# Optimization experiments

Measured on AMD Instinct MI355X. Metric: run time of the kernel, lower is better.

Reference implementation:

```python
import jax, jax.numpy as jnp
import numpy as np

V, E, H, A, S, B = 32000, 1024, 1024, 10, 512, 64


def setup_inputs() -> dict:
    key = jax.random.key(0)
    ks = jax.random.split(key, 12)
    s = 0.02
    return {
        "dec_input": jax.random.randint(ks[0], (B, 1), 0, V, dtype=jnp.int32),
        "dec_hidden": jax.random.normal(ks[1], (1, B, H), jnp.float32),
        "enc_outputs": jax.random.normal(ks[2], (S, B, H), jnp.float32),
        "emb": jax.random.normal(ks[3], (V, E), jnp.float32) * s,
        "Wa1": jax.random.normal(ks[4], (A, 2 * H), jnp.float32) * s,  # attention layer 1, no bias
        "Wa2": jax.random.normal(ks[5], (1, A), jnp.float32) * s,      # attention layer 2, no bias
        "W_ih": jax.random.normal(ks[6], (3 * H, E + H), jnp.float32) * s,  # GRU input weights (r,z,n)
        "W_hh": jax.random.normal(ks[7], (3 * H, H), jnp.float32) * s,      # GRU hidden weights (r,z,n)
        "b_ih": jnp.zeros((3 * H,), jnp.float32),
        "b_hh": jnp.zeros((3 * H,), jnp.float32),
        "W_out": jax.random.normal(ks[8], (V, H), jnp.float32) * s,
        "b_out": jnp.zeros((V,), jnp.float32),
    }


def reference(dec_input, dec_hidden, enc_outputs, emb, Wa1, Wa2, W_ih, W_hh, b_ih, b_hh, W_out, b_out):
    h_last = dec_hidden[-1]  # [B, H]
    # Bahdanau additive attention over encoder time steps (axis 0)
    hh = jnp.broadcast_to(h_last[None], enc_outputs.shape)        # [S, B, H]
    feats = jnp.concatenate([hh, enc_outputs], axis=-1)           # [S, B, 2H]
    e = jnp.tanh(feats @ Wa1.T) @ Wa2.T                           # [S, B, 1]
    alpha = jax.nn.softmax(e, axis=0)                             # softmax over seq
    c = jnp.sum(alpha * enc_outputs, axis=0)                      # [B, H]
    # embedding lookup for the single decoder step
    x = emb[dec_input[:, 0]]                                      # [B, E]
    xc = jnp.concatenate([x, c], axis=1)                          # [B, E+H]
    # single-step GRU (PyTorch gate order: r, z, n)
    gi = xc @ W_ih.T + b_ih                                       # [B, 3H]
    gh = h_last @ W_hh.T + b_hh                                   # [B, 3H]
    i_r, i_z, i_n = jnp.split(gi, 3, axis=1)
    h_r, h_z, h_n = jnp.split(gh, 3, axis=1)
    r = jax.nn.sigmoid(i_r + h_r)
    z = jax.nn.sigmoid(i_z + h_z)
    n = jnp.tanh(i_n + r * h_n)
    h_new = (1.0 - z) * n + z * h_last                            # [B, H]
    logits = h_new @ W_out.T + b_out                              # [B, V]
    return logits, h_new[None]                                    # ([B,V], [1,B,H])
```

## Files before the change

kernel.cpp:

```cpp
#include <hip/hip_runtime.h>
#include <math.h>

#define Vv 32000
#define Ee 1024
#define Hh 1024
#define Aa 10
#define Ss 512
#define Bb 64

typedef __attribute__((ext_vector_type(8))) short bf16x8;
typedef __attribute__((ext_vector_type(4))) short s16x4;
typedef __attribute__((ext_vector_type(4))) float f32x4;

__device__ inline short f2bf(float f) {
    union { float f; unsigned int u; } v;
    v.f = f;
    unsigned int r = (v.u + 0x7FFFu + ((v.u >> 16) & 1u)) >> 16;
    return (short)r;
}

__device__ inline bf16x8 cvt8(float4 lo, float4 hi) {
    bf16x8 r;
    r[0] = f2bf(lo.x); r[1] = f2bf(lo.y); r[2] = f2bf(lo.z); r[3] = f2bf(lo.w);
    r[4] = f2bf(hi.x); r[5] = f2bf(hi.y); r[6] = f2bf(hi.z); r[7] = f2bf(hi.w);
    return r;
}

__global__ __launch_bounds__(256) void hpart_kernel(const float* __restrict__ Wa1,
                                                    const float* __restrict__ h,
                                                    float* __restrict__ hpart) {
    __shared__ float red[256];
    const int b = blockIdx.x, t = threadIdx.x;
    float p[Aa];
#pragma unroll
    for (int a = 0; a < Aa; a++) p[a] = 0.f;
    for (int k = t; k < Hh; k += 256) {
        float hv = h[b * Hh + k];
#pragma unroll
        for (int a = 0; a < Aa; a++) p[a] += Wa1[a * (2 * Hh) + k] * hv;
    }
    for (int a = 0; a < Aa; a++) {
        red[t] = p[a];
        __syncthreads();
        for (int o = 128; o > 0; o >>= 1) {
            if (t < o) red[t] += red[t + o];
            __syncthreads();
        }
        if (t == 0) hpart[b * 16 + a] = red[0];
        __syncthreads();
    }
}

__global__ __launch_bounds__(256) void scores_kernel(const float* __restrict__ enc,
                                                     const float* __restrict__ Wa1,
                                                     const float* __restrict__ Wa2,
                                                     const float* __restrict__ hpart,
                                                     float* __restrict__ e_out) {
    __shared__ float es[64][65];
    __shared__ float red[4][64][11];
    const int t = threadIdx.x;
    const int m0 = blockIdx.x * 64;
    const int q = __builtin_amdgcn_readfirstlane((int)(t >> 6));
    const int lane = t & 63;
    const float4* enc4 = (const float4*)enc;

    float acc[Aa];
#pragma unroll
    for (int a = 0; a < Aa; a++) acc[a] = 0.f;

    for (int c = 0; c < 16; c++) {
#pragma unroll
        for (int p = 0; p < 4; p++) {
            int idx = t + p * 256;
            int r = idx >> 4, kq = idx & 15;
            float4 v = enc4[(size_t)(m0 + r) * 256 + c * 16 + kq];
            es[r][kq * 4 + 0] = v.x;
            es[r][kq * 4 + 1] = v.y;
            es[r][kq * 4 + 2] = v.z;
            es[r][kq * 4 + 3] = v.w;
        }
        __syncthreads();
        const int kbase = Hh + c * 64 + q * 16;
#pragma unroll
        for (int j = 0; j < 16; j++) {
            float ev = es[lane][q * 16 + j];
#pragma unroll
            for (int a = 0; a < Aa; a++)
                acc[a] += Wa1[a * (2 * Hh) + kbase + j] * ev;
        }
        __syncthreads();
    }
#pragma unroll
    for (int a = 0; a < Aa; a++) red[q][lane][a] = acc[a];
    __syncthreads();
    if (t < 64) {
        float ev = 0.f;
#pragma unroll
        for (int a = 0; a < Aa; a++) {
            float tot = red[0][t][a] + red[1][t][a] + red[2][t][a] + red[3][t][a]
                        + hpart[t * 16 + a];
            ev += Wa2[a] * tanhf(tot);
        }
        e_out[m0 + t] = ev;
    }
}

__global__ __launch_bounds__(512) void softmax_kernel(const float* __restrict__ e,
                                                      float* __restrict__ alpha) {
    __shared__ float red[512];
    const int b = blockIdx.x, s = threadIdx.x;
    float v = e[s * Bb + b];
    red[s] = v;
    __syncthreads();
    for (int o = 256; o > 0; o >>= 1) {
        if (s < o) red[s] = fmaxf(red[s], red[s + o]);
        __syncthreads();
    }
    float m = red[0];
    __syncthreads();
    float ex = expf(v - m);
    red[s] = ex;
    __syncthreads();
    for (int o = 256; o > 0; o >>= 1) {
        if (s < o) red[s] += red[s + o];
        __syncthreads();
    }
    float inv = 1.f / red[0];
    alpha[s * Bb + b] = ex * inv;
}

__global__ __launch_bounds__(128) void context_kernel(const float* __restrict__ enc,
                                                      const float* __restrict__ alpha,
                                                      float* __restrict__ c) {
    const int b = blockIdx.x, hc = blockIdx.y, sc = blockIdx.z;
    const int h4 = hc * 128 + threadIdx.x;
    const float4* enc4 = (const float4*)enc;
    float4 acc = {0.f, 0.f, 0.f, 0.f};
    const int s0 = sc * 128;
    for (int s = s0; s < s0 + 128; ++s) {
        float a = alpha[s * Bb + b];
        float4 ev = enc4[(size_t)(s * Bb + b) * 256 + h4];
        acc.x += a * ev.x;
        acc.y += a * ev.y;
        acc.z += a * ev.z;
        acc.w += a * ev.w;
    }
    float* cp = c + b * Hh + h4 * 4;
    atomicAdd(cp + 0, acc.x);
    atomicAdd(cp + 1, acc.y);
    atomicAdd(cp + 2, acc.z);
    atomicAdd(cp + 3, acc.w);
}

__global__ __launch_bounds__(256) void xc_kernel(const int* __restrict__ dec_input,
                                                 const float* __restrict__ emb,
                                                 const float* __restrict__ c,
                                                 const float* __restrict__ h,
                                                 short* __restrict__ xcb,
                                                 short* __restrict__ hb) {
    const int b = blockIdx.x, t = threadIdx.x;
    const int tok = dec_input[b];
    float4 ev = ((const float4*)(emb + (size_t)tok * Ee))[t];
    float4 cv = ((const float4*)(c + (size_t)b * Hh))[t];
    float4 hv = ((const float4*)(h + (size_t)b * Hh))[t];
    s16x4 e4 = {f2bf(ev.x), f2bf(ev.y), f2bf(ev.z), f2bf(ev.w)};
    s16x4 c4 = {f2bf(cv.x), f2bf(cv.y), f2bf(cv.z), f2bf(cv.w)};
    s16x4 h4 = {f2bf(hv.x), f2bf(hv.y), f2bf(hv.z), f2bf(hv.w)};
    ((s16x4*)(xcb + (size_t)b * 2048))[t] = e4;
    ((s16x4*)(xcb + (size_t)b * 2048 + 1024))[t] = c4;
    ((s16x4*)(hb + (size_t)b * 1024))[t] = h4;
}

__global__ __launch_bounds__(256) void gemm_mfma_kernel(
    const short* __restrict__ Abf,
    const float* __restrict__ W,
    const float* __restrict__ bias,
    float* __restrict__ C,
    int N, int K, int Klen, int doAtomic) {
    const int t = threadIdx.x;
    const int w = t >> 6, lane = t & 63;
    const int col = lane & 15, quad = lane >> 4;
    const int n0 = blockIdx.x * 64 + w * 16;
    const int kb0 = blockIdx.y * Klen;

    f32x4 acc[4];
#pragma unroll
    for (int mt = 0; mt < 4; mt++) acc[mt] = (f32x4){0.f, 0.f, 0.f, 0.f};

    const float* wrow = W + (size_t)(n0 + col) * K + kb0 + quad * 8;
    const short* arow = Abf + (size_t)col * K + kb0 + quad * 8;

    for (int kb = 0; kb < Klen; kb += 64) {
        float4 w0 = *(const float4*)(wrow + kb);
        float4 w1 = *(const float4*)(wrow + kb + 4);
        float4 w2 = *(const float4*)(wrow + kb + 32);
        float4 w3 = *(const float4*)(wrow + kb + 36);
        bf16x8 bf0 = cvt8(w0, w1);
        bf16x8 bf1 = cvt8(w2, w3);
        bf16x8 a0[4], a1[4];
#pragma unroll
        for (int mt = 0; mt < 4; mt++) {
            a0[mt] = *(const bf16x8*)(arow + (size_t)mt * 16 * K + kb);
            a1[mt] = *(const bf16x8*)(arow + (size_t)mt * 16 * K + kb + 32);
        }
#pragma unroll
        for (int mt = 0; mt < 4; mt++)
            acc[mt] = __builtin_amdgcn_mfma_f32_16x16x32_bf16(a0[mt], bf0, acc[mt], 0, 0, 0);
#pragma unroll
        for (int mt = 0; mt < 4; mt++)
            acc[mt] = __builtin_amdgcn_mfma_f32_16x16x32_bf16(a1[mt], bf1, acc[mt], 0, 0, 0);
    }

    const float bv = (bias != nullptr) ? bias[n0 + col] : 0.f;
#pragma unroll
    for (int mt = 0; mt < 4; mt++) {
#pragma unroll
        for (int r = 0; r < 4; r++) {
            int m = mt * 16 + quad * 4 + r;
            size_t off = (size_t)m * N + n0 + col;
            if (doAtomic) atomicAdd(&C[off], acc[mt][r]);
            else C[off] = acc[mt][r] + bv;
        }
    }
}

__global__ __launch_bounds__(256) void gru_kernel(const float* __restrict__ gi,
                                                  const float* __restrict__ gh,
                                                  const float* __restrict__ b_ih,
                                                  const float* __restrict__ b_hh,
                                                  const float* __restrict__ h,
                                                  float* __restrict__ h_new,
                                                  short* __restrict__ hnb) {
    const int idx = blockIdx.x * 256 + threadIdx.x;
    const int b = idx >> 10, j = idx & 1023;
    const size_t base = (size_t)b * (3 * Hh);
    float ir = gi[base + j] + b_ih[j];
    float iz = gi[base + Hh + j] + b_ih[Hh + j];
    float in_ = gi[base + 2 * Hh + j] + b_ih[2 * Hh + j];
    float hr = gh[base + j] + b_hh[j];
    float hz = gh[base + Hh + j] + b_hh[Hh + j];
    float hn = gh[base + 2 * Hh + j] + b_hh[2 * Hh + j];
    float r = 1.f / (1.f + expf(-(ir + hr)));
    float z = 1.f / (1.f + expf(-(iz + hz)));
    float n = tanhf(in_ + r * hn);
    float val = (1.f - z) * n + z * h[idx];
    h_new[idx] = val;
    hnb[idx] = f2bf(val);
}

extern "C" void kernel_launch(void* const* d_in, const int* in_sizes, int n_in,
                              void* d_out, int out_size, void* d_ws, size_t ws_size,
                              hipStream_t stream) {
    const int* dec_input = (const int*)d_in[0];
    const float* dec_hidden = (const float*)d_in[1];
    const float* enc = (const float*)d_in[2];
    const float* emb = (const float*)d_in[3];
    const float* Wa1 = (const float*)d_in[4];
    const float* Wa2 = (const float*)d_in[5];
    const float* W_ih = (const float*)d_in[6];
    const float* W_hh = (const float*)d_in[7];
    const float* b_ih = (const float*)d_in[8];
    const float* b_hh = (const float*)d_in[9];
    const float* W_out = (const float*)d_in[10];
    const float* b_out = (const float*)d_in[11];

    float* out = (float*)d_out;
    float* logits = out;
    float* h_new = out + (size_t)Bb * Vv;

    float* ws = (float*)d_ws;
    float* e_ptr = ws;
    float* alpha_ptr = ws + 32768;
    float* hpart_ptr = ws + 65536;
    float* c_ptr = ws + 66560;
    float* gi_ptr = ws + 132096;
    float* gh_ptr = ws + 328704;
    short* xcb_ptr = (short*)(ws + 525312);
    short* hb_ptr = (short*)(ws + 590848);
    short* hnb_ptr = (short*)(ws + 623616);

    hipMemsetAsync(c_ptr, 0, (size_t)Bb * Hh * sizeof(float), stream);
    hipMemsetAsync(gi_ptr, 0, (size_t)2 * Bb * 3 * Hh * sizeof(float), stream);

    hpart_kernel<<<Bb, 256, 0, stream>>>(Wa1, dec_hidden, hpart_ptr);
    scores_kernel<<<(Ss * Bb) / 64, 256, 0, stream>>>(enc, Wa1, Wa2, hpart_ptr, e_ptr);
    softmax_kernel<<<Bb, 512, 0, stream>>>(e_ptr, alpha_ptr);
    context_kernel<<<dim3(Bb, 2, 4), 128, 0, stream>>>(enc, alpha_ptr, c_ptr);
    xc_kernel<<<Bb, 256, 0, stream>>>(dec_input, emb, c_ptr, dec_hidden, xcb_ptr, hb_ptr);

    gemm_mfma_kernel<<<dim3(3 * Hh / 64, 8), 256, 0, stream>>>(
        xcb_ptr, W_ih, nullptr, gi_ptr, 3 * Hh, Ee + Hh, 256, 1);
    gemm_mfma_kernel<<<dim3(3 * Hh / 64, 4), 256, 0, stream>>>(
        hb_ptr, W_hh, nullptr, gh_ptr, 3 * Hh, Hh, 256, 1);

    gru_kernel<<<(Bb * Hh) / 256, 256, 0, stream>>>(gi_ptr, gh_ptr, b_ih, b_hh,
                                                    dec_hidden, h_new, hnb_ptr);

    gemm_mfma_kernel<<<dim3(Vv / 64, 1), 256, 0, stream>>>(
        hnb_ptr, W_out, b_out, logits, Vv, Hh, 1024, 0);
}
```

Measured before the change: 481.6 us.

## Use MFMA for attention scores and replace atomics with split-K partial buffers

The attention score projection (enc @ Wa1 encoder half) now runs on bf16 MFMA with two K-splits, and the tanh/Wa2 combine moves into the softmax kernel. Context and GRU GEMMs write split partials to workspace buffers instead of using atomicAdd, so the memsets go away and the reductions happen in xc_kernel and gru_kernel. The aim is to cut the scalar FMA cost of the scores pass and the atomic traffic, at the cost of bf16 rounding in the scores, extra partial-buffer reads, and workspace regions reused across stages.

Result: faster. 448.0 us (-7.0%).

```diff
diff --git a/kernel.cpp b/kernel.cpp
--- a/kernel.cpp
+++ b/kernel.cpp
@@ -7,6 +7,7 @@
 #define Aa 10
 #define Ss 512
 #define Bb 64
+#define Mm (Ss * Bb)
 
 typedef __attribute__((ext_vector_type(8))) short bf16x8;
 typedef __attribute__((ext_vector_type(4))) short s16x4;
@@ -51,74 +52,67 @@
     }
 }
 
-__global__ __launch_bounds__(256) void scores_kernel(const float* __restrict__ enc,
-                                                     const float* __restrict__ Wa1,
-                                                     const float* __restrict__ Wa2,
-                                                     const float* __restrict__ hpart,
-                                                     float* __restrict__ e_out) {
-    __shared__ float es[64][65];
-    __shared__ float red[4][64][11];
+__global__ __launch_bounds__(256) void scores_mfma_kernel(
+    const float* __restrict__ enc,
+    const float* __restrict__ Wa1,
+    float* __restrict__ epre) {
     const int t = threadIdx.x;
-    const int m0 = blockIdx.x * 64;
-    const int q = __builtin_amdgcn_readfirstlane((int)(t >> 6));
-    const int lane = t & 63;
-    const float4* enc4 = (const float4*)enc;
-
-    float acc[Aa];
-#pragma unroll
-    for (int a = 0; a < Aa; a++) acc[a] = 0.f;
-
+    const int w = t >> 6, lane = t & 63;
+    const int col = lane & 15, quad = lane >> 4;
+    const int m0 = (blockIdx.x * 4 + w) * 16;
+    const int p = blockIdx.y;
+    const int kb0 = p * 512;
+
+    f32x4 acc = {0.f, 0.f, 0.f, 0.f};
+    const int wa_row = (col < Aa) ? col : 0;
+    const float* wrow = Wa1 + (size_t)wa_row * (2 * Hh) + Hh + kb0 + quad * 8;
+    const float* arow = enc + (size_t)(m0 + col) * Hh + kb0 + quad * 8;
+    const bool valid = (col < Aa);
+
+#pragma unroll
     for (int c = 0; c < 16; c++) {
-#pragma unroll
-        for (int p = 0; p < 4; p++) {
-            int idx = t + p * 256;
-            int r = idx >> 4, kq = idx & 15;
-            float4 v = enc4[(size_t)(m0 + r) * 256 + c * 16 + kq];
-            es[r][kq * 4 + 0] = v.x;
-            es[r][kq * 4 + 1] = v.y;
-            es[r][kq * 4 + 2] = v.z;
-            es[r][kq * 4 + 3] = v.w;
+        float4 a0 = *(const float4*)(arow + c * 32);
+        float4 a1 = *(const float4*)(arow + c * 32 + 4);
+        bf16x8 af = cvt8(a0, a1);
+        bf16x8 bf;
+        if (valid) {
+            float4 b0 = *(const float4*)(wrow + c * 32);
+            float4 b1 = *(const float4*)(wrow + c * 32 + 4);
+            bf = cvt8(b0, b1);
+        } else {
+            bf = (bf16x8){0, 0, 0, 0, 0, 0, 0, 0};
         }
-        __syncthreads();
-        const int kbase = Hh + c * 64 + q * 16;
-#pragma unroll
-        for (int j = 0; j < 16; j++) {
-            float ev = es[lane][q * 16 + j];
-#pragma unroll
-            for (int a = 0; a < Aa; a++)
-                acc[a] += Wa1[a * (2 * Hh) + kbase + j] * ev;
-        }
-        __syncthreads();
-    }
-#pragma unroll
-    for (int a = 0; a < Aa; a++) red[q][lane][a] = acc[a];
-    __syncthreads();
-    if (t < 64) {
-        float ev = 0.f;
-#pragma unroll
-        for (int a = 0; a < Aa; a++) {
-            float tot = red[0][t][a] + red[1][t][a] + red[2][t][a] + red[3][t][a]
-                        + hpart[t * 16 + a];
-            ev += Wa2[a] * tanhf(tot);
-        }
-        e_out[m0 + t] = ev;
-    }
-}
-
-__global__ __launch_bounds__(512) void softmax_kernel(const float* __restrict__ e,
+        acc = __builtin_amdgcn_mfma_f32_16x16x32_bf16(af, bf, acc, 0, 0, 0);
+    }
+    float* out = epre + ((size_t)p * Mm + m0) * 16;
+#pragma unroll
+    for (int r = 0; r < 4; r++)
+        out[(quad * 4 + r) * 16 + col] = acc[r];
+}
+
+__global__ __launch_bounds__(512) void softmax_kernel(const float* __restrict__ epre,
+                                                      const float* __restrict__ hpart,
+                                                      const float* __restrict__ Wa2,
                                                       float* __restrict__ alpha) {
     __shared__ float red[512];
     const int b = blockIdx.x, s = threadIdx.x;
-    float v = e[s * Bb + b];
+    const int m = s * Bb + b;
+    float v = 0.f;
+#pragma unroll
+    for (int a = 0; a < Aa; a++) {
+        float tot = hpart[b * 16 + a] + epre[(size_t)m * 16 + a]
+                    + epre[((size_t)Mm + m) * 16 + a];
+        v += Wa2[a] * tanhf(tot);
+    }
     red[s] = v;
     __syncthreads();
     for (int o = 256; o > 0; o >>= 1) {
         if (s < o) red[s] = fmaxf(red[s], red[s + o]);
         __syncthreads();
     }
-    float m = red[0];
+    float mx = red[0];
     __syncthreads();
-    float ex = expf(v - m);
+    float ex = expf(v - mx);
     red[s] = ex;
     __syncthreads();
     for (int o = 256; o > 0; o >>= 1) {
@@ -129,15 +123,15 @@
     alpha[s * Bb + b] = ex * inv;
 }
 
-__global__ __launch_bounds__(128) void context_kernel(const float* __restrict__ enc,
+__global__ __launch_bounds__(256) void context_kernel(const float* __restrict__ enc,
                                                       const float* __restrict__ alpha,
-                                                      float* __restrict__ c) {
-    const int b = blockIdx.x, hc = blockIdx.y, sc = blockIdx.z;
-    const int h4 = hc * 128 + threadIdx.x;
+                                                      float* __restrict__ cpart) {
+    const int b = blockIdx.x, sc = blockIdx.y;
+    const int h4 = threadIdx.x;
     const float4* enc4 = (const float4*)enc;
     float4 acc = {0.f, 0.f, 0.f, 0.f};
-    const int s0 = sc * 128;
-    for (int s = s0; s < s0 + 128; ++s) {
+    const int s0 = sc * 32;
+    for (int s = s0; s < s0 + 32; ++s) {
         float a = alpha[s * Bb + b];
         float4 ev = enc4[(size_t)(s * Bb + b) * 256 + h4];
         acc.x += a * ev.x;
@@ -145,30 +139,31 @@
         acc.z += a * ev.z;
         acc.w += a * ev.w;
     }
-    float* cp = c + b * Hh + h4 * 4;
-    atomicAdd(cp + 0, acc.x);
-    atomicAdd(cp + 1, acc.y);
-    atomicAdd(cp + 2, acc.z);
-    atomicAdd(cp + 3, acc.w);
+    ((float4*)cpart)[((size_t)sc * Bb + b) * 256 + h4] = acc;
 }
 
 __global__ __launch_bounds__(256) void xc_kernel(const int* __restrict__ dec_input,
                                                  const float* __restrict__ emb,
-                                                 const float* __restrict__ c,
+                                                 const float* __restrict__ cpart,
                                                  const float* __restrict__ h,
                                                  short* __restrict__ xcb,
                                                  short* __restrict__ hb) {
     const int b = blockIdx.x, t = threadIdx.x;
     const int tok = dec_input[b];
+    float4 cv = {0.f, 0.f, 0.f, 0.f};
+#pragma unroll
+    for (int p = 0; p < 16; p++) {
+        float4 v = ((const float4*)cpart)[((size_t)p * Bb + b) * 256 + t];
+        cv.x += v.x; cv.y += v.y; cv.z += v.z; cv.w += v.w;
+    }
     float4 ev = ((const float4*)(emb + (size_t)tok * Ee))[t];
-    float4 cv = ((const float4*)(c + (size_t)b * Hh))[t];
     float4 hv = ((const float4*)(h + (size_t)b * Hh))[t];
     s16x4 e4 = {f2bf(ev.x), f2bf(ev.y), f2bf(ev.z), f2bf(ev.w)};
     s16x4 c4 = {f2bf(cv.x), f2bf(cv.y), f2bf(cv.z), f2bf(cv.w)};
-    s16x4 h4 = {f2bf(hv.x), f2bf(hv.y), f2bf(hv.z), f2bf(hv.w)};
+    s16x4 h4v = {f2bf(hv.x), f2bf(hv.y), f2bf(hv.z), f2bf(hv.w)};
     ((s16x4*)(xcb + (size_t)b * 2048))[t] = e4;
     ((s16x4*)(xcb + (size_t)b * 2048 + 1024))[t] = c4;
-    ((s16x4*)(hb + (size_t)b * 1024))[t] = h4;
+    ((s16x4*)(hb + (size_t)b * 1024))[t] = h4v;
 }
 
 __global__ __launch_bounds__(256) void gemm_mfma_kernel(
@@ -176,7 +171,7 @@
     const float* __restrict__ W,
     const float* __restrict__ bias,
     float* __restrict__ C,
-    int N, int K, int Klen, int doAtomic) {
+    int N, int K, int Klen) {
     const int t = threadIdx.x;
     const int w = t >> 6, lane = t & 63;
     const int col = lane & 15, quad = lane >> 4;
@@ -212,20 +207,19 @@
     }
 
     const float bv = (bias != nullptr) ? bias[n0 + col] : 0.f;
+    float* Cp = C + (size_t)blockIdx.y * 64 * N;
 #pragma unroll
     for (int mt = 0; mt < 4; mt++) {
 #pragma unroll
         for (int r = 0; r < 4; r++) {
             int m = mt * 16 + quad * 4 + r;
-            size_t off = (size_t)m * N + n0 + col;
-            if (doAtomic) atomicAdd(&C[off], acc[mt][r]);
-            else C[off] = acc[mt][r] + bv;
+            Cp[(size_t)m * N + n0 + col] = acc[mt][r] + bv;
         }
     }
 }
 
-__global__ __launch_bounds__(256) void gru_kernel(const float* __restrict__ gi,
-                                                  const float* __restrict__ gh,
+__global__ __launch_bounds__(256) void gru_kernel(const float* __restrict__ gip,
+                                                  const float* __restrict__ ghp,
                                                   const float* __restrict__ b_ih,
                                                   const float* __restrict__ b_hh,
                                                   const float* __restrict__ h,
@@ -234,12 +228,18 @@
     const int idx = blockIdx.x * 256 + threadIdx.x;
     const int b = idx >> 10, j = idx & 1023;
     const size_t base = (size_t)b * (3 * Hh);
-    float ir = gi[base + j] + b_ih[j];
-    float iz = gi[base + Hh + j] + b_ih[Hh + j];
-    float in_ = gi[base + 2 * Hh + j] + b_ih[2 * Hh + j];
-    float hr = gh[base + j] + b_hh[j];
-    float hz = gh[base + Hh + j] + b_hh[Hh + j];
-    float hn = gh[base + 2 * Hh + j] + b_hh[2 * Hh + j];
+    float ir = b_ih[j], iz = b_ih[Hh + j], in_ = b_ih[2 * Hh + j];
+    float hr = b_hh[j], hz = b_hh[Hh + j], hn = b_hh[2 * Hh + j];
+#pragma unroll
+    for (int p = 0; p < 8; p++) {
+        const float* g = gip + (size_t)p * Bb * 3 * Hh + base;
+        ir += g[j]; iz += g[Hh + j]; in_ += g[2 * Hh + j];
+    }
+#pragma unroll
+    for (int p = 0; p < 8; p++) {
+        const float* g = ghp + (size_t)p * Bb * 3 * Hh + base;
+        hr += g[j]; hz += g[Hh + j]; hn += g[2 * Hh + j];
+    }
     float r = 1.f / (1.f + expf(-(ir + hr)));
     float z = 1.f / (1.f + expf(-(iz + hz)));
     float n = tanhf(in_ + r * hn);
@@ -269,33 +269,33 @@
     float* h_new = out + (size_t)Bb * Vv;
 
     float* ws = (float*)d_ws;
-    float* e_ptr = ws;
-    float* alpha_ptr = ws + 32768;
-    float* hpart_ptr = ws + 65536;
-    float* c_ptr = ws + 66560;
-    float* gi_ptr = ws + 132096;
-    float* gh_ptr = ws + 328704;
-    short* xcb_ptr = (short*)(ws + 525312);
-    short* hb_ptr = (short*)(ws + 590848);
-    short* hnb_ptr = (short*)(ws + 623616);
-
-    hipMemsetAsync(c_ptr, 0, (size_t)Bb * Hh * sizeof(float), stream);
-    hipMemsetAsync(gi_ptr, 0, (size_t)2 * Bb * 3 * Hh * sizeof(float), stream);
+    float* alpha_ptr = ws;
+    float* hpart_ptr = ws + 32768;
+    short* xcb_ptr = (short*)(ws + 33792);
+    short* hb_ptr = (short*)(ws + 99328);
+    short* hnb_ptr = (short*)(ws + 132096);
+    float* region1 = ws + 164864;
+    float* region2 = ws + 1737728;
+    float* epre_ptr = region1;
+    float* gip_ptr = region1;
+    float* cpart_ptr = region2;
+    float* ghp_ptr = region2;
 
     hpart_kernel<<<Bb, 256, 0, stream>>>(Wa1, dec_hidden, hpart_ptr);
-    scores_kernel<<<(Ss * Bb) / 64, 256, 0, stream>>>(enc, Wa1, Wa2, hpart_ptr, e_ptr);
-    softmax_kernel<<<Bb, 512, 0, stream>>>(e_ptr, alpha_ptr);
-    context_kernel<<<dim3(Bb, 2, 4), 128, 0, stream>>>(enc, alpha_ptr, c_ptr);
-    xc_kernel<<<Bb, 256, 0, stream>>>(dec_input, emb, c_ptr, dec_hidden, xcb_ptr, hb_ptr);
+    scores_mfma_kernel<<<dim3(Mm / 64, 2), 256, 0, stream>>>(enc, Wa1, epre_ptr);
+    softmax_kernel<<<Bb, 512, 0, stream>>>(epre_ptr, hpart_ptr, Wa2, alpha_ptr);
+    context_kernel<<<dim3(Bb, 16), 256, 0, stream>>>(enc, alpha_ptr, cpart_ptr);
+    xc_kernel<<<Bb, 256, 0, stream>>>(dec_input, emb, cpart_ptr, dec_hidden,
+                                      xcb_ptr, hb_ptr);
 
     gemm_mfma_kernel<<<dim3(3 * Hh / 64, 8), 256, 0, stream>>>(
-        xcb_ptr, W_ih, nullptr, gi_ptr, 3 * Hh, Ee + Hh, 256, 1);
-    gemm_mfma_kernel<<<dim3(3 * Hh / 64, 4), 256, 0, stream>>>(
-        hb_ptr, W_hh, nullptr, gh_ptr, 3 * Hh, Hh, 256, 1);
-
-    gru_kernel<<<(Bb * Hh) / 256, 256, 0, stream>>>(gi_ptr, gh_ptr, b_ih, b_hh,
+        xcb_ptr, W_ih, nullptr, gip_ptr, 3 * Hh, Ee + Hh, 256);
+    gemm_mfma_kernel<<<dim3(3 * Hh / 64, 8), 256, 0, stream>>>(
+        hb_ptr, W_hh, nullptr, ghp_ptr, 3 * Hh, Hh, 128);
+
+    gru_kernel<<<(Bb * Hh) / 256, 256, 0, stream>>>(gip_ptr, ghp_ptr, b_ih, b_hh,
                                                     dec_hidden, h_new, hnb_ptr);
 
     gemm_mfma_kernel<<<dim3(Vv / 64, 1), 256, 0, stream>>>(
-        hnb_ptr, W_out, b_out, logits, Vv, Hh, 1024, 0);
-}
+        hnb_ptr, W_out, b_out, logits, Vv, Hh, 1024);
+}
```
